# Optimization experiments

Measured on AMD Instinct MI355X. Metric: run time of the kernel, lower is better.

## Reference

```python
import jax, jax.numpy as jnp
import numpy as np

B, N, NF, EF, L = 32, 100, 128, 128, 3
ALPHA = 0.3  # keras LeakyReLU default


def _affine_act(h, W, S, Bb):
    # 1x1 conv (no bias) + folded BatchNorm (scale S, shift Bb) + LeakyReLU
    return jax.nn.leaky_relu(h @ W * S + Bb, ALPHA)


def _node_update(node_feat, edge_feat, W0, S0, B0, W1, S1, B1):
    n = node_feat.shape[1]
    dmask = (1.0 - jnp.eye(n, dtype=node_feat.dtype))[None, None]  # [1,1,N,N]
    ef = edge_feat * dmask
    norms = jnp.sum(jnp.abs(ef), axis=-1, keepdims=True)  # L1 norm
    ef = jnp.where(norms == 0, 0.0, ef / jnp.where(norms == 0, 1.0, norms))
    aggr = jnp.einsum('bemn,bnd->bemd', ef, node_feat)          # [B,2,N,D]
    aggr = jnp.concatenate([aggr[:, 0], aggr[:, 1]], axis=-1)   # [B,N,2D]
    x = jnp.concatenate([node_feat, aggr], axis=-1)             # [B,N,3D]
    h = _affine_act(x, W0, S0, B0)
    return _affine_act(h, W1, S1, B1)


def _edge_update(node_feat, edge_feat, convs, Wout, bout):
    n = node_feat.shape[1]
    # pairwise abs-diff: [B,N,N,F]
    h = jnp.abs(node_feat[:, :, None, :] - node_feat[:, None, :, :])
    for W, S, Bb in convs:
        h = _affine_act(h, W, S, Bb)
    sim = jax.nn.sigmoid(h @ Wout + bout)          # [B,N,N]
    sims = jnp.stack([sim, 1.0 - sim], axis=1)     # [B,2,N,N]
    eye = jnp.eye(n, dtype=node_feat.dtype)
    ef = edge_feat * (1.0 - eye)[None, None]
    merge_sum = jnp.sum(ef, axis=-1, keepdims=True)
    ef = ef * sims
    norms = jnp.sum(jnp.abs(ef), axis=-1, keepdims=True)
    ef = jnp.where(norms == 0, 0.0, ef / jnp.where(norms == 0, 1.0, norms))
    ef = ef * merge_sum
    force = jnp.stack([eye, jnp.zeros_like(eye)], axis=0)[None]  # [1,2,N,N]
    ef = ef + force + 1e-6
    return ef / jnp.sum(ef, axis=1, keepdims=True)


def setup_inputs() -> dict:
    key = jax.random.key(0)
    ks = jax.random.split(key, 10)
    f32 = jnp.float32

    def w(k, shape):
        return (jax.random.normal(k, shape, f32) * 0.05).astype(f32)

    d = {}
    d['node_feat'] = jax.random.normal(ks[0], (B, N, NF), f32)
    d['edge_feat'] = jax.random.uniform(ks[1], (B, 2, N, N), dtype=f32)
    # node-update MLP (ratio [2,1]): in 3*NF -> 2*NF -> NF
    d['nW0'] = w(ks[2], (L, 3 * NF, 2 * NF)); d['nS0'] = jnp.ones((L, 2 * NF), f32); d['nB0'] = jnp.zeros((L, 2 * NF), f32)
    d['nW1'] = w(ks[3], (L, 2 * NF, NF));     d['nS1'] = jnp.ones((L, NF), f32);     d['nB1'] = jnp.zeros((L, NF), f32)
    # edge sim network (ratio [2,2,1,1]): NF -> 2EF -> 2EF -> EF -> EF -> 1
    d['eW0'] = w(ks[4], (L, NF, 2 * EF));     d['eS0'] = jnp.ones((L, 2 * EF), f32); d['eB0'] = jnp.zeros((L, 2 * EF), f32)
    d['eW1'] = w(ks[5], (L, 2 * EF, 2 * EF)); d['eS1'] = jnp.ones((L, 2 * EF), f32); d['eB1'] = jnp.zeros((L, 2 * EF), f32)
    d['eW2'] = w(ks[6], (L, 2 * EF, EF));     d['eS2'] = jnp.ones((L, EF), f32);     d['eB2'] = jnp.zeros((L, EF), f32)
    d['eW3'] = w(ks[7], (L, EF, EF));         d['eS3'] = jnp.ones((L, EF), f32);     d['eB3'] = jnp.zeros((L, EF), f32)
    d['eWout'] = w(ks[8], (L, EF));           d['eBout'] = jnp.zeros((L,), f32)
    return d


def reference(node_feat, edge_feat, nW0, nS0, nB0, nW1, nS1, nB1,
              eW0, eS0, eB0, eW1, eS1, eB1, eW2, eS2, eB2, eW3, eS3, eB3,
              eWout, eBout):
    nf, ef = node_feat, edge_feat
    for l in range(L):
        nf = _node_update(nf, ef, nW0[l], nS0[l], nB0[l], nW1[l], nS1[l], nB1[l])
        convs = [(eW0[l], eS0[l], eB0[l]), (eW1[l], eS1[l], eB1[l]),
                 (eW2[l], eS2[l], eB2[l]), (eW3[l], eS3[l], eB3[l])]
        ef = _edge_update(nf, ef, convs, eWout[l], eBout[l])
    return ef
```

## Files before the change

### kernel.cpp

```cpp
#include <hip/hip_runtime.h>
#include <math.h>

#define ALPHA 0.3f

constexpr int B  = 32;
constexpr int N  = 100;
constexpr int NF = 128;
constexpr int L  = 3;
constexpr int NN = N * N;
constexpr int NTRI = N * (N + 1) / 2;
constexpr int NPAIR_TRI = B * NTRI;
constexpr int PT = 80;
constexpr int RT = 32;

typedef __attribute__((ext_vector_type(8))) short short8;
typedef __attribute__((ext_vector_type(4))) float f32x4;

__device__ __forceinline__ unsigned short f2bf(float x) {
    union { float f; unsigned u; } v; v.f = x;
    unsigned r = v.u + 0x7FFF + ((v.u >> 16) & 1);
    return (unsigned short)(r >> 16);
}
__device__ __forceinline__ float bf2f(unsigned short h) {
    union { unsigned u; float f; } v; v.u = ((unsigned)h) << 16;
    return v.f;
}
__device__ __forceinline__ unsigned cvt_pk(float lo, float hi) {
    unsigned r;
    asm("v_cvt_pk_bf16_f32 %0, %1, %2" : "=v"(r) : "v"(lo), "v"(hi));
    return r;
}

__device__ __forceinline__ void tri_decode(int t, int& io, int& jo) {
    int ii = (int)((201.0f - sqrtf(40401.0f - 8.0f * (float)t)) * 0.5f);
    ii = max(0, min(99, ii));
    while (ii > 0 && ii * (201 - ii) / 2 > t) --ii;
    while ((ii + 1) * (200 - ii) / 2 <= t) ++ii;
    io = ii;
    jo = ii + (t - ii * (201 - ii) / 2);
}

__device__ __forceinline__ void wprep_elem(const float* __restrict__ W,
                                           const float* __restrict__ S,
                                           unsigned short* __restrict__ Wp,
                                           int K, int C, int idx) {
    const int per = K * C;
    const int l = idx / per, r = idx - l * per;
    const int KS = K / 32;
    const int j    = r & 7;
    const int lane = (r >> 3) & 63;
    const int t2   = r >> 9;
    const int ks = t2 % KS, ct = t2 / KS;
    const int c = ct * 16 + (lane & 15);
    const int k = ks * 32 + (lane >> 4) * 8 + j;
    float v = W[(size_t)l * per + (size_t)k * C + c] * S[l * C + c];
    Wp[idx] = f2bf(v);
}

constexpr int SEG0 = L * 128 * 256;
constexpr int SEG1 = L * 256 * 256;
constexpr int SEG2 = L * 256 * 128;
constexpr int SEG3 = L * 128 * 128;
constexpr int SEG4 = L * 384 * 256;
constexpr int SEG5 = L * 256 * 128;
constexpr int PREP_TOTAL = SEG0 + SEG1 + SEG2 + SEG3 + SEG4 + SEG5 + NTRI;

__global__ void k_prep_all(
    const float* __restrict__ eW0, const float* __restrict__ eS0, unsigned short* __restrict__ w0t,
    const float* __restrict__ eW1, const float* __restrict__ eS1, unsigned short* __restrict__ w1t,
    const float* __restrict__ eW2, const float* __restrict__ eS2, unsigned short* __restrict__ w2t,
    const float* __restrict__ eW3, const float* __restrict__ eS3, unsigned short* __restrict__ w3t,
    const float* __restrict__ nW0, const float* __restrict__ nS0, unsigned short* __restrict__ nw0f,
    const float* __restrict__ nW1, const float* __restrict__ nS1, unsigned short* __restrict__ nw1f,
    unsigned* __restrict__ tab) {
    int idx = blockIdx.x * 256 + threadIdx.x;
    if (idx < SEG0) { wprep_elem(eW0, eS0, w0t, 128, 256, idx); return; }
    idx -= SEG0;
    if (idx < SEG1) { wprep_elem(eW1, eS1, w1t, 256, 256, idx); return; }
    idx -= SEG1;
    if (idx < SEG2) { wprep_elem(eW2, eS2, w2t, 256, 128, idx); return; }
    idx -= SEG2;
    if (idx < SEG3) { wprep_elem(eW3, eS3, w3t, 128, 128, idx); return; }
    idx -= SEG3;
    if (idx < SEG4) { wprep_elem(nW0, nS0, nw0f, 384, 256, idx); return; }
    idx -= SEG4;
    if (idx < SEG5) { wprep_elem(nW1, nS1, nw1f, 256, 128, idx); return; }
    idx -= SEG5;
    if (idx < NTRI) {
        int i, j;
        tri_decode(idx, i, j);
        tab[idx] = (unsigned)((i << 8) | j);
    }
}

__global__ void k_aggr_x(const float* __restrict__ nf,
                         const float* __restrict__ ef,
                         float* __restrict__ x) {
    const int b = blockIdx.x / N;
    const int m = blockIdx.x - b * N;
    const int t = threadIdx.x;

    __shared__ float w0[128], w1[128];

    float e0 = 0.f, e1 = 0.f;
    if (t < N) {
        e0 = ef[((size_t)(b * 2 + 0) * N + m) * N + t];
        e1 = ef[((size_t)(b * 2 + 1) * N + m) * N + t];
        if (t == m) { e0 = 0.f; e1 = 0.f; }
    }
    w0[t] = fabsf(e0);
    w1[t] = fabsf(e1);
    __syncthreads();
    for (int s = 64; s > 0; s >>= 1) {
        if (t < s) { w0[t] += w0[t + s]; w1[t] += w1[t + s]; }
        __syncthreads();
    }
    const float s0 = w0[0];
    const float s1 = w1[0];
    __syncthreads();
    w0[t] = (s0 == 0.f) ? 0.f : e0 / s0;
    w1[t] = (s1 == 0.f) ? 0.f : e1 / s1;
    __syncthreads();

    const float* nfb = nf + (size_t)b * N * NF;
    float a0 = 0.f, a1 = 0.f;
#pragma unroll 4
    for (int n = 0; n < N; ++n) {
        const float v = nfb[(size_t)n * NF + t];
        a0 = fmaf(w0[n], v, a0);
        a1 = fmaf(w1[n], v, a1);
    }
    float* xr = x + (size_t)(b * N + m) * (3 * NF);
    xr[t]          = nfb[(size_t)m * NF + t];
    xr[NF + t]     = a0;
    xr[2 * NF + t] = a1;
}

template <int K, int NT>
__device__ __forceinline__ void load_bv0(const unsigned short* __restrict__ Wf,
                                         int lane, int wave, short8* bv) {
    constexpr int KS = K / 32;
#pragma unroll
    for (int n = 0; n < NT; ++n)
        bv[n] = *(const short8*)(Wf + (((size_t)(wave * NT + n) * KS) * 64 + lane) * 8);
}

template <int K, int COUT, int NT, int MT>
__device__ __forceinline__ void layer_mfma(const unsigned short* in,
                                           unsigned short* out,
                                           const unsigned short* __restrict__ Wf,
                                           const float* __restrict__ Bb,
                                           int lane, int wave, const short8* bv0) {
    constexpr int KS = K / 32;
    const int r16 = lane & 15, g = lane >> 4;
    f32x4 acc[MT][NT];
#pragma unroll
    for (int n = 0; n < NT; ++n) {
        const f32x4 binit = *(const f32x4*)(Bb + (wave * NT + n) * 16 + g * 4);
#pragma unroll
        for (int m = 0; m < MT; ++m) acc[m][n] = binit;
    }

#pragma unroll
    for (int ks = 0; ks < KS; ++ks) {
        short8 av[MT];
        const int abyte = (ks * 64 + g * 16) ^ (r16 << 4);
#pragma unroll
        for (int m = 0; m < MT; ++m) {
            const int p = m * 16 + r16;
            av[m] = *(const short8*)((const char*)in + p * (K * 2) + abyte);
        }
        short8 bv[NT];
#pragma unroll
        for (int n = 0; n < NT; ++n) {
            if (ks == 0) bv[n] = bv0[n];
            else bv[n] = *(const short8*)(Wf + (((size_t)(wave * NT + n) * KS + ks) * 64 + lane) * 8);
        }
#pragma unroll
        for (int m = 0; m < MT; ++m)
#pragma unroll
            for (int n = 0; n < NT; ++n)
                acc[m][n] = __builtin_amdgcn_mfma_f32_16x16x32_bf16(
                    bv[n], av[m], acc[m][n], 0, 0, 0);
    }
#pragma unroll
    for (int n = 0; n < NT; ++n) {
        const int c0 = wave * NT * 16 + n * 16 + g * 4;
#pragma unroll
        for (int m = 0; m < MT; ++m) {
            const int p = m * 16 + r16;
            float v0 = acc[m][n][0]; v0 = fmaxf(v0, ALPHA * v0);
            float v1 = acc[m][n][1]; v1 = fmaxf(v1, ALPHA * v1);
            float v2 = acc[m][n][2]; v2 = fmaxf(v2, ALPHA * v2);
            float v3 = acc[m][n][3]; v3 = fmaxf(v3, ALPHA * v3);
            uint2 w;
            w.x = cvt_pk(v0, v1);
            w.y = cvt_pk(v2, v3);
            const int byte = (c0 * 2) ^ (r16 << 4);
            *(uint2*)((char*)out + p * (COUT * 2) + byte) = w;
        }
    }
}

template <int K, int MT>
__device__ __forceinline__ void layer_mfma_sim(const unsigned short* in,
                                               float* __restrict__ psum,
                                               const unsigned short* __restrict__ Wf,
                                               const float* __restrict__ Bb,
                                               const float* __restrict__ Wout,
                                               int lane, int wave, short8 bv0) {
    constexpr int KS = K / 32;
    const int r16 = lane & 15, g = lane >> 4;
    f32x4 acc[MT];
    {
        const f32x4 binit = *(const f32x4*)(Bb + wave * 16 + g * 4);
#pragma unroll
        for (int m = 0; m < MT; ++m) acc[m] = binit;
    }

#pragma unroll
    for (int ks = 0; ks < KS; ++ks) {
        short8 av[MT];
        const int abyte = (ks * 64 + g * 16) ^ (r16 << 4);
#pragma unroll
        for (int m = 0; m < MT; ++m) {
            const int p = m * 16 + r16;
            av[m] = *(const short8*)((const char*)in + p * (K * 2) + abyte);
        }
        const short8 bv = (ks == 0) ? bv0
            : *(const short8*)(Wf + (((size_t)wave * KS + ks) * 64 + lane) * 8);
#pragma unroll
        for (int m = 0; m < MT; ++m)
            acc[m] = __builtin_amdgcn_mfma_f32_16x16x32_bf16(bv, av[m], acc[m], 0, 0, 0);
    }

    const float4 w4 = *(const float4*)(Wout + wave * 16 + g * 4);
#pragma unroll
    for (int m = 0; m < MT; ++m) {
        float v0 = acc[m][0]; v0 = fmaxf(v0, ALPHA * v0);
        float v1 = acc[m][1]; v1 = fmaxf(v1, ALPHA * v1);
        float v2 = acc[m][2]; v2 = fmaxf(v2, ALPHA * v2);
        float v3 = acc[m][3]; v3 = fmaxf(v3, ALPHA * v3);
        float part = v0 * w4.x;
        part = fmaf(v1, w4.y, part);
        part = fmaf(v2, w4.z, part);
        part = fmaf(v3, w4.w, part);
        part += __shfl_xor(part, 16);
        part += __shfl_xor(part, 32);
        if (g == 0) psum[wave * (MT * 16) + m * 16 + r16] = part;
    }
}

template <int K, int COUT, int NT, int MT>
__device__ __forceinline__ void layer_mfma_f32out(const unsigned short* in,
                                                  float* __restrict__ outg, int row0,
                                                  const unsigned short* __restrict__ Wf,
                                                  const float* __restrict__ Bb,
                                                  int lane, int wave, const short8* bv0) {
    constexpr int KS = K / 32;
    const int r16 = lane & 15, g = lane >> 4;
    f32x4 acc[MT][NT];
#pragma unroll
    for (int n = 0; n < NT; ++n) {
        const f32x4 binit = *(const f32x4*)(Bb + (wave * NT + n) * 16 + g * 4);
#pragma unroll
        for (int m = 0; m < MT; ++m) acc[m][n] = binit;
    }

#pragma unroll
    for (int ks = 0; ks < KS; ++ks) {
        short8 av[MT];
        const int abyte = (ks * 64 + g * 16) ^ (r16 << 4);
#pragma unroll
        for (int m = 0; m < MT; ++m) {
            const int p = m * 16 + r16;
            av[m] = *(const short8*)((const char*)in + p * (K * 2) + abyte);
        }
        short8 bv[NT];
#pragma unroll
        for (int n = 0; n < NT; ++n) {
            if (ks == 0) bv[n] = bv0[n];
            else bv[n] = *(const short8*)(Wf + (((size_t)(wave * NT + n) * KS + ks) * 64 + lane) * 8);
        }
#pragma unroll
        for (int m = 0; m < MT; ++m)
#pragma unroll
            for (int n = 0; n < NT; ++n)
                acc[m][n] = __builtin_amdgcn_mfma_f32_16x16x32_bf16(
                    bv[n], av[m], acc[m][n], 0, 0, 0);
    }
#pragma unroll
    for (int n = 0; n < NT; ++n) {
        const int c0 = wave * NT * 16 + n * 16 + g * 4;
#pragma unroll
        for (int m = 0; m < MT; ++m) {
            const int p = m * 16 + r16;
            float4 o;
            o.x = acc[m][n][0]; o.x = fmaxf(o.x, ALPHA * o.x);
            o.y = acc[m][n][1]; o.y = fmaxf(o.y, ALPHA * o.y);
            o.z = acc[m][n][2]; o.z = fmaxf(o.z, ALPHA * o.z);
            o.w = acc[m][n][3]; o.w = fmaxf(o.w, ALPHA * o.w);
            *(float4*)(outg + (size_t)(row0 + p) * COUT + c0) = o;
        }
    }
}

__global__ __launch_bounds__(512, 4) void k_node_mfma(
    const float* __restrict__ x,
    const unsigned short* __restrict__ W0f, const float* __restrict__ B0,
    const unsigned short* __restrict__ W1f, const float* __restrict__ B1,
    float* __restrict__ nf_out) {
    __shared__ unsigned short bufA[RT * 384];
    __shared__ unsigned short bufB[RT * 256];
    const int t = threadIdx.x;
    const int lane = t & 63, wave = t >> 6;
    const int row0 = blockIdx.x * RT;

    {
        const int p = t >> 4, q = t & 15;
        const float* xr = x + (size_t)(row0 + p) * 384;
#pragma unroll
        for (int u = 0; u < 3; ++u) {
            const int q8 = q + u * 16;
            const float4 a0 = *(const float4*)(xr + q8 * 8);
            const float4 a1 = *(const float4*)(xr + q8 * 8 + 4);
            uint4 o;
            o.x = cvt_pk(a0.x, a0.y);
            o.y = cvt_pk(a0.z, a0.w);
            o.z = cvt_pk(a1.x, a1.y);
            o.w = cvt_pk(a1.z, a1.w);
            const int byte = (q8 * 16) ^ ((p & 15) << 4);
            *(uint4*)((char*)bufA + p * 768 + byte) = o;
        }
    }
    short8 bvp[2];
    load_bv0<384, 2>(W0f, lane, wave, bvp);
    __syncthreads();
    layer_mfma<384, 256, 2, 2>(bufA, bufB, W0f, B0, lane, wave, bvp);
    load_bv0<256, 1>(W1f, lane, wave, bvp);
    __syncthreads();
    layer_mfma_f32out<256, 128, 1, 2>(bufB, nf_out, row0, W1f, B1, lane, wave, bvp);
}

__global__ __launch_bounds__(512, 4) void k_pair_mlp_mfma(
    const float* __restrict__ nf,
    const unsigned short* __restrict__ W0f, const float* __restrict__ Bb0,
    const unsigned short* __restrict__ W1f, const float* __restrict__ Bb1,
    const unsigned short* __restrict__ W2f, const float* __restrict__ Bb2,
    const unsigned short* __restrict__ W3f, const float* __restrict__ Bb3,
    const float* __restrict__ Wout, const float* __restrict__ boutp,
    const unsigned* __restrict__ tab,
    float* __restrict__ sim) {
    __shared__ unsigned short bufA[PT * 256];
    __shared__ unsigned short bufB[PT * 256];
    const int t = threadIdx.x;
    const int lane = t & 63, wave = t >> 6;
    const int tile0 = blockIdx.x * PT;

    {
        const int p0 = t >> 4, q = t & 15;
        for (int p = p0; p < PT; p += 32) {
            const int P = tile0 + p;
            const int b = P / NTRI;
            const unsigned ij = tab[P - b * NTRI];
            const int i = ij >> 8, j = ij & 255;
            const float4* fi = (const float4*)(nf + ((size_t)(b * N + i)) * NF + q * 8);
            const float4* fj = (const float4*)(nf + ((size_t)(b * N + j)) * NF + q * 8);
            const float4 a0 = fi[0], a1 = fi[1];
            const float4 c0 = fj[0], c1 = fj[1];
            uint4 o;
            o.x = cvt_pk(fabsf(a0.x - c0.x), fabsf(a0.y - c0.y));
            o.y = cvt_pk(fabsf(a0.z - c0.z), fabsf(a0.w - c0.w));
            o.z = cvt_pk(fabsf(a1.x - c1.x), fabsf(a1.y - c1.y));
            o.w = cvt_pk(fabsf(a1.z - c1.z), fabsf(a1.w - c1.w));
            const int byte = (q * 16) ^ ((p & 15) << 4);
            *(uint4*)((char*)bufA + p * 256 + byte) = o;
        }
    }
    short8 bvp[2];
    load_bv0<128, 2>(W0f, lane, wave, bvp);
    __syncthreads();
    layer_mfma<128, 256, 2, 5>(bufA, bufB, W0f, Bb0, lane, wave, bvp);
    load_bv0<256, 2>(W1f, lane, wave, bvp);
    __syncthreads();
    layer_mfma<256, 256, 2, 5>(bufB, bufA, W1f, Bb1, lane, wave, bvp);
    load_bv0<256, 1>(W2f, lane, wave, bvp);
    __syncthreads();
    layer_mfma<256, 128, 1, 5>(bufA, bufB, W2f, Bb2, lane, wave, bvp);
    load_bv0<128, 1>(W3f, lane, wave, bvp);
    __syncthreads();
    float* psum = (float*)bufA;
    layer_mfma_sim<128, 5>(bufB, psum, W3f, Bb3, Wout, lane, wave, bvp[0]);
    __syncthreads();

    if (t < PT) {
        float acc = 0.f;
#pragma unroll
        for (int w = 0; w < 8; ++w) acc += psum[w * PT + t];
        const int P = tile0 + t;
        const int b = P / NTRI;
        const unsigned ij = tab[P - b * NTRI];
        const int i = ij >> 8, j = ij & 255;
        const float v = acc + boutp[0];
        const float sv = 1.f / (1.f + expf(-v));
        sim[((size_t)(b * N) + i) * N + j] = sv;
        sim[((size_t)(b * N) + j) * N + i] = sv;
    }
}

__global__ void k_edge_update(const float* __restrict__ ef_in,
                              const float* __restrict__ sim,
                              float* __restrict__ ef_out) {
    const int b = blockIdx.x / N;
    const int i = blockIdx.x - b * N;
    const int t = threadIdx.x;

    __shared__ float r0[128], r1[128], r2[128], r3[128];

    float e0 = 0.f, e1 = 0.f, s = 0.f;
    if (t < N) {
        e0 = ef_in[((size_t)(b * 2 + 0) * N + i) * N + t];
        e1 = ef_in[((size_t)(b * 2 + 1) * N + i) * N + t];
        if (t == i) { e0 = 0.f; e1 = 0.f; }
        s = sim[(size_t)(b * N + i) * N + t];
    }
    float f0 = e0 * s;
    float f1 = e1 * (1.f - s);
    r0[t] = e0; r1[t] = e1; r2[t] = fabsf(f0); r3[t] = fabsf(f1);
    __syncthreads();
    for (int st = 64; st > 0; st >>= 1) {
        if (t < st) {
            r0[t] += r0[t + st];
            r1[t] += r1[t + st];
            r2[t] += r2[t + st];
            r3[t] += r3[t + st];
        }
        __syncthreads();
    }
    const float m0 = r0[0], m1 = r1[0], n0 = r2[0], n1 = r3[0];
    if (t < N) {
        f0 = (n0 == 0.f) ? 0.f : (f0 / n0) * m0;
        f1 = (n1 == 0.f) ? 0.f : (f1 / n1) * m1;
        if (t == i) f0 += 1.f;
        f0 += 1e-6f;
        f1 += 1e-6f;
        const float inv = 1.f / (f0 + f1);
        ef_out[((size_t)(b * 2 + 0) * N + i) * N + t] = f0 * inv;
        ef_out[((size_t)(b * 2 + 1) * N + i) * N + t] = f1 * inv;
    }
}

__global__ void k_edge_aggr(const float* __restrict__ ef_in,
                            const float* __restrict__ sim,
                            const float* __restrict__ nf,
                            float* __restrict__ ef_out,
                            float* __restrict__ x) {
    const int b = blockIdx.x / N;
    const int i = blockIdx.x - b * N;
    const int t = threadIdx.x;

    __shared__ float r0[128], r1[128], r2[128], r3[128];
    __shared__ float w0s[128], w1s[128];

    float e0 = 0.f, e1 = 0.f, s = 0.f;
    if (t < N) {
        e0 = ef_in[((size_t)(b * 2 + 0) * N + i) * N + t];
        e1 = ef_in[((size_t)(b * 2 + 1) * N + i) * N + t];
        if (t == i) { e0 = 0.f; e1 = 0.f; }
        s = sim[(size_t)(b * N + i) * N + t];
    }
    float f0 = e0 * s;
    float f1 = e1 * (1.f - s);
    r0[t] = e0; r1[t] = e1; r2[t] = fabsf(f0); r3[t] = fabsf(f1);
    __syncthreads();
    for (int st = 64; st > 0; st >>= 1) {
        if (t < st) {
            r0[t] += r0[t + st];
            r1[t] += r1[t + st];
            r2[t] += r2[t + st];
            r3[t] += r3[t + st];
        }
        __syncthreads();
    }
    const float m0 = r0[0], m1 = r1[0], n0 = r2[0], n1 = r3[0];
    float g0 = 0.f, g1 = 0.f;
    if (t < N) {
        f0 = (n0 == 0.f) ? 0.f : (f0 / n0) * m0;
        f1 = (n1 == 0.f) ? 0.f : (f1 / n1) * m1;
        if (t == i) f0 += 1.f;
        f0 += 1e-6f;
        f1 += 1e-6f;
        const float inv = 1.f / (f0 + f1);
        g0 = f0 * inv;
        g1 = f1 * inv;
        ef_out[((size_t)(b * 2 + 0) * N + i) * N + t] = g0;
        ef_out[((size_t)(b * 2 + 1) * N + i) * N + t] = g1;
    }

    const float a0in = (t < N && t != i) ? g0 : 0.f;
    const float a1in = (t < N && t != i) ? g1 : 0.f;
    __syncthreads();
    r0[t] = fabsf(a0in);
    r1[t] = fabsf(a1in);
    __syncthreads();
    for (int st = 64; st > 0; st >>= 1) {
        if (t < st) { r0[t] += r0[t + st]; r1[t] += r1[t + st]; }
        __syncthreads();
    }
    const float s0 = r0[0], s1 = r1[0];
    __syncthreads();
    w0s[t] = (s0 == 0.f) ? 0.f : a0in / s0;
    w1s[t] = (s1 == 0.f) ? 0.f : a1in / s1;
    __syncthreads();

    const float* nfb = nf + (size_t)b * N * NF;
    float a0 = 0.f, a1 = 0.f;
#pragma unroll 4
    for (int n = 0; n < N; ++n) {
        const float v = nfb[(size_t)n * NF + t];
        a0 = fmaf(w0s[n], v, a0);
        a1 = fmaf(w1s[n], v, a1);
    }
    float* xr = x + (size_t)(b * N + i) * (3 * NF);
    xr[t]          = nfb[(size_t)i * NF + t];
    xr[NF + t]     = a0;
    xr[2 * NF + t] = a1;
}

extern "C" void kernel_launch(void* const* d_in, const int* in_sizes, int n_in,
                              void* d_out, int out_size, void* d_ws, size_t ws_size,
                              hipStream_t stream) {
    (void)in_sizes; (void)n_in; (void)out_size; (void)ws_size;

    const float* node_feat = (const float*)d_in[0];
    const float* edge_feat = (const float*)d_in[1];
    const float* nW0 = (const float*)d_in[2];
    const float* nS0 = (const float*)d_in[3];
    const float* nB0 = (const float*)d_in[4];
    const float* nW1 = (const float*)d_in[5];
    const float* nS1 = (const float*)d_in[6];
    const float* nB1 = (const float*)d_in[7];
    const float* eW0 = (const float*)d_in[8];
    const float* eS0 = (const float*)d_in[9];
    const float* eB0 = (const float*)d_in[10];
    const float* eW1 = (const float*)d_in[11];
    const float* eS1 = (const float*)d_in[12];
    const float* eB1 = (const float*)d_in[13];
    const float* eW2 = (const float*)d_in[14];
    const float* eS2 = (const float*)d_in[15];
    const float* eB2 = (const float*)d_in[16];
    const float* eW3 = (const float*)d_in[17];
    const float* eS3 = (const float*)d_in[18];
    const float* eB3 = (const float*)d_in[19];
    const float* eWout = (const float*)d_in[20];
    const float* eBout = (const float*)d_in[21];

    float* ws     = (float*)d_ws;
    float* nf_a   = ws;
    float* nf_b   = nf_a + (size_t)B * N * NF;
    float* xbuf   = nf_b + (size_t)B * N * NF;
    float* ef_ws  = xbuf + (size_t)B * N * 3 * NF;
    float* simbuf = ef_ws + (size_t)B * 2 * N * N;
    unsigned short* w0t = (unsigned short*)(simbuf + (size_t)B * N * N);
    unsigned short* w1t = w0t + (size_t)L * 256 * 128;
    unsigned short* w2t = w1t + (size_t)L * 256 * 256;
    unsigned short* w3t = w2t + (size_t)L * 128 * 256;
    unsigned short* nw0f = w3t + (size_t)L * 128 * 128;
    unsigned short* nw1f = nw0f + (size_t)L * 256 * 384;
    unsigned* tab = (unsigned*)(nw1f + (size_t)L * 128 * 256);

    k_prep_all<<<(PREP_TOTAL + 255) / 256, 256, 0, stream>>>(
        eW0, eS0, w0t, eW1, eS1, w1t, eW2, eS2, w2t, eW3, eS3, w3t,
        nW0, nS0, nw0f, nW1, nS1, nw1f, tab);

    const float* ef_cur = edge_feat;
    float* nf_next_buf[3] = {nf_a, nf_b, nf_a};

    k_aggr_x<<<B * N, 128, 0, stream>>>(node_feat, edge_feat, xbuf);

    for (int l = 0; l < L; ++l) {
        k_node_mfma<<<B * N / RT, 512, 0, stream>>>(
            xbuf,
            nw0f + (size_t)l * 256 * 384, nB0 + l * 2 * NF,
            nw1f + (size_t)l * 128 * 256, nB1 + l * NF,
            nf_next_buf[l]);
        const float* nf_cur = nf_next_buf[l];

        k_pair_mlp_mfma<<<NPAIR_TRI / PT, 512, 0, stream>>>(
            nf_cur,
            w0t + (size_t)l * 256 * 128, eB0 + l * 256,
            w1t + (size_t)l * 256 * 256, eB1 + l * 256,
            w2t + (size_t)l * 128 * 256, eB2 + l * 128,
            w3t + (size_t)l * 128 * 128, eB3 + l * 128,
            eWout + (size_t)l * 128, eBout + l, tab, simbuf);

        if (l < L - 1) {
            k_edge_aggr<<<B * N, 128, 0, stream>>>(
                ef_cur, simbuf, nf_cur, ef_ws, xbuf);
            ef_cur = ef_ws;
        } else {
            k_edge_update<<<B * N, 128, 0, stream>>>(ef_cur, simbuf, (float*)d_out);
        }
    }
}
```

Measured before the change: 229.9 us.

## Retile pair-MLP waves into a 2x4 grid and shrink the pair tile

The pair MLP kernel now handles 64 pairs per block instead of 80. Its 8 waves form a 2x4 grid over row and column tiles, where each wave previously covered all row tiles for a slice of output columns. Each wave now reads fewer activation fragments from LDS but more weight fragments from global memory, and the final sigmoid reduction is reworked to sum over column-wave partials. The smaller tile lowers LDS use and gives exactly divisible blocks, but weight-load traffic per MFMA goes up.

```diff
diff --git a/kernel.cpp b/kernel.cpp
--- a/kernel.cpp
+++ b/kernel.cpp
@@ -10,7 +10,7 @@
 constexpr int NN = N * N;
 constexpr int NTRI = N * (N + 1) / 2;
 constexpr int NPAIR_TRI = B * NTRI;
-constexpr int PT = 80;
+constexpr int PT = 64;
 constexpr int RT = 32;
 
 typedef __attribute__((ext_vector_type(8))) short short8;
@@ -138,11 +138,11 @@
 
 template <int K, int NT>
 __device__ __forceinline__ void load_bv0(const unsigned short* __restrict__ Wf,
-                                         int lane, int wave, short8* bv) {
+                                         int lane, int ct0, short8* bv) {
     constexpr int KS = K / 32;
 #pragma unroll
     for (int n = 0; n < NT; ++n)
-        bv[n] = *(const short8*)(Wf + (((size_t)(wave * NT + n) * KS) * 64 + lane) * 8);
+        bv[n] = *(const short8*)(Wf + (((size_t)(ct0 + n) * KS) * 64 + lane) * 8);
 }
 
 template <int K, int COUT, int NT, int MT>
@@ -150,13 +150,14 @@
                                            unsigned short* out,
                                            const unsigned short* __restrict__ Wf,
                                            const float* __restrict__ Bb,
-                                           int lane, int wave, const short8* bv0) {
+                                           int lane, int mbase, int ct0,
+                                           const short8* bv0) {
     constexpr int KS = K / 32;
     const int r16 = lane & 15, g = lane >> 4;
     f32x4 acc[MT][NT];
 #pragma unroll
     for (int n = 0; n < NT; ++n) {
-        const f32x4 binit = *(const f32x4*)(Bb + (wave * NT + n) * 16 + g * 4);
+        const f32x4 binit = *(const f32x4*)(Bb + (ct0 + n) * 16 + g * 4);
 #pragma unroll
         for (int m = 0; m < MT; ++m) acc[m][n] = binit;
     }
@@ -167,14 +168,14 @@
         const int abyte = (ks * 64 + g * 16) ^ (r16 << 4);
 #pragma unroll
         for (int m = 0; m < MT; ++m) {
-            const int p = m * 16 + r16;
+            const int p = (mbase + m) * 16 + r16;
             av[m] = *(const short8*)((const char*)in + p * (K * 2) + abyte);
         }
         short8 bv[NT];
 #pragma unroll
         for (int n = 0; n < NT; ++n) {
             if (ks == 0) bv[n] = bv0[n];
-            else bv[n] = *(const short8*)(Wf + (((size_t)(wave * NT + n) * KS + ks) * 64 + lane) * 8);
+            else bv[n] = *(const short8*)(Wf + (((size_t)(ct0 + n) * KS + ks) * 64 + lane) * 8);
         }
 #pragma unroll
         for (int m = 0; m < MT; ++m)
@@ -185,10 +186,10 @@
     }
 #pragma unroll
     for (int n = 0; n < NT; ++n) {
-        const int c0 = wave * NT * 16 + n * 16 + g * 4;
+        const int c0 = (ct0 + n) * 16 + g * 4;
 #pragma unroll
         for (int m = 0; m < MT; ++m) {
-            const int p = m * 16 + r16;
+            const int p = (mbase + m) * 16 + r16;
             float v0 = acc[m][n][0]; v0 = fmaxf(v0, ALPHA * v0);
             float v1 = acc[m][n][1]; v1 = fmaxf(v1, ALPHA * v1);
             float v2 = acc[m][n][2]; v2 = fmaxf(v2, ALPHA * v2);
@@ -202,20 +203,22 @@
     }
 }
 
-template <int K, int MT>
+template <int K, int NT, int MT>
 __device__ __forceinline__ void layer_mfma_sim(const unsigned short* in,
                                                float* __restrict__ psum,
                                                const unsigned short* __restrict__ Wf,
                                                const float* __restrict__ Bb,
                                                const float* __restrict__ Wout,
-                                               int lane, int wave, short8 bv0) {
+                                               int lane, int mbase, int ct0, int wave,
+                                               const short8* bv0) {
     constexpr int KS = K / 32;
     const int r16 = lane & 15, g = lane >> 4;
-    f32x4 acc[MT];
-    {
-        const f32x4 binit = *(const f32x4*)(Bb + wave * 16 + g * 4);
-#pragma unroll
-        for (int m = 0; m < MT; ++m) acc[m] = binit;
+    f32x4 acc[MT][NT];
+#pragma unroll
+    for (int n = 0; n < NT; ++n) {
+        const f32x4 binit = *(const f32x4*)(Bb + (ct0 + n) * 16 + g * 4);
+#pragma unroll
+        for (int m = 0; m < MT; ++m) acc[m][n] = binit;
     }
 
 #pragma unroll
@@ -224,27 +227,41 @@
         const int abyte = (ks * 64 + g * 16) ^ (r16 << 4);
 #pragma unroll
         for (int m = 0; m < MT; ++m) {
-            const int p = m * 16 + r16;
+            const int p = (mbase + m) * 16 + r16;
             av[m] = *(const short8*)((const char*)in + p * (K * 2) + abyte);
         }
-        const short8 bv = (ks == 0) ? bv0
-            : *(const short8*)(Wf + (((size_t)wave * KS + ks) * 64 + lane) * 8);
+        short8 bv[NT];
+#pragma unroll
+        for (int n = 0; n < NT; ++n) {
+            if (ks == 0) bv[n] = bv0[n];
+            else bv[n] = *(const short8*)(Wf + (((size_t)(ct0 + n) * KS + ks) * 64 + lane) * 8);
+        }
 #pragma unroll
         for (int m = 0; m < MT; ++m)
-            acc[m] = __builtin_amdgcn_mfma_f32_16x16x32_bf16(bv, av[m], acc[m], 0, 0, 0);
-    }
-
-    const float4 w4 = *(const float4*)(Wout + wave * 16 + g * 4);
+#pragma unroll
+            for (int n = 0; n < NT; ++n)
+                acc[m][n] = __builtin_amdgcn_mfma_f32_16x16x32_bf16(
+                    bv[n], av[m], acc[m][n], 0, 0, 0);
+    }
+
+    float4 w4[NT];
+#pragma unroll
+    for (int n = 0; n < NT; ++n)
+        w4[n] = *(const float4*)(Wout + (ct0 + n) * 16 + g * 4);
 #pragma unroll
     for (int m = 0; m < MT; ++m) {
-        float v0 = acc[m][0]; v0 = fmaxf(v0, ALPHA * v0);
-        float v1 = acc[m][1]; v1 = fmaxf(v1, ALPHA * v1);
-        float v2 = acc[m][2]; v2 = fmaxf(v2, ALPHA * v2);
-        float v3 = acc[m][3]; v3 = fmaxf(v3, ALPHA * v3);
-        float part = v0 * w4.x;
-        part = fmaf(v1, w4.y, part);
-        part = fmaf(v2, w4.z, part);
-        part = fmaf(v3, w4.w, part);
+        float part = 0.f;
+#pragma unroll
+        for (int n = 0; n < NT; ++n) {
+            float v0 = acc[m][n][0]; v0 = fmaxf(v0, ALPHA * v0);
+            float v1 = acc[m][n][1]; v1 = fmaxf(v1, ALPHA * v1);
+            float v2 = acc[m][n][2]; v2 = fmaxf(v2, ALPHA * v2);
+            float v3 = acc[m][n][3]; v3 = fmaxf(v3, ALPHA * v3);
+            part = fmaf(v0, w4[n].x, part);
+            part = fmaf(v1, w4[n].y, part);
+            part = fmaf(v2, w4[n].z, part);
+            part = fmaf(v3, w4[n].w, part);
+        }
         part += __shfl_xor(part, 16);
         part += __shfl_xor(part, 32);
         if (g == 0) psum[wave * (MT * 16) + m * 16 + r16] = part;
@@ -256,13 +273,14 @@
                                                   float* __restrict__ outg, int row0,
                                                   const unsigned short* __restrict__ Wf,
                                                   const float* __restrict__ Bb,
-                                                  int lane, int wave, const short8* bv0) {
+                                                  int lane, int mbase, int ct0,
+                                                  const short8* bv0) {
     constexpr int KS = K / 32;
     const int r16 = lane & 15, g = lane >> 4;
     f32x4 acc[MT][NT];
 #pragma unroll
     for (int n = 0; n < NT; ++n) {
-        const f32x4 binit = *(const f32x4*)(Bb + (wave * NT + n) * 16 + g * 4);
+        const f32x4 binit = *(const f32x4*)(Bb + (ct0 + n) * 16 + g * 4);
 #pragma unroll
         for (int m = 0; m < MT; ++m) acc[m][n] = binit;
     }
@@ -273,14 +291,14 @@
         const int abyte = (ks * 64 + g * 16) ^ (r16 << 4);
 #pragma unroll
         for (int m = 0; m < MT; ++m) {
-            const int p = m * 16 + r16;
+            const int p = (mbase + m) * 16 + r16;
             av[m] = *(const short8*)((const char*)in + p * (K * 2) + abyte);
         }
         short8 bv[NT];
 #pragma unroll
         for (int n = 0; n < NT; ++n) {
             if (ks == 0) bv[n] = bv0[n];
-            else bv[n] = *(const short8*)(Wf + (((size_t)(wave * NT + n) * KS + ks) * 64 + lane) * 8);
+            else bv[n] = *(const short8*)(Wf + (((size_t)(ct0 + n) * KS + ks) * 64 + lane) * 8);
         }
 #pragma unroll
         for (int m = 0; m < MT; ++m)
@@ -291,10 +309,10 @@
     }
 #pragma unroll
     for (int n = 0; n < NT; ++n) {
-        const int c0 = wave * NT * 16 + n * 16 + g * 4;
+        const int c0 = (ct0 + n) * 16 + g * 4;
 #pragma unroll
         for (int m = 0; m < MT; ++m) {
-            const int p = m * 16 + r16;
+            const int p = (mbase + m) * 16 + r16;
             float4 o;
             o.x = acc[m][n][0]; o.x = fmaxf(o.x, ALPHA * o.x);
             o.y = acc[m][n][1]; o.y = fmaxf(o.y, ALPHA * o.y);
@@ -333,13 +351,13 @@
             *(uint4*)((char*)bufA + p * 768 + byte) = o;
         }
     }
-    short8 bvp[2];
-    load_bv0<384, 2>(W0f, lane, wave, bvp);
-    __syncthreads();
-    layer_mfma<384, 256, 2, 2>(bufA, bufB, W0f, B0, lane, wave, bvp);
+    short8 bvp[4];
+    load_bv0<384, 2>(W0f, lane, wave * 2, bvp);
+    __syncthreads();
+    layer_mfma<384, 256, 2, 2>(bufA, bufB, W0f, B0, lane, 0, wave * 2, bvp);
     load_bv0<256, 1>(W1f, lane, wave, bvp);
     __syncthreads();
-    layer_mfma_f32out<256, 128, 1, 2>(bufB, nf_out, row0, W1f, B1, lane, wave, bvp);
+    layer_mfma_f32out<256, 128, 1, 2>(bufB, nf_out, row0, W1f, B1, lane, 0, wave, bvp);
 }
 
 __global__ __launch_bounds__(512, 4) void k_pair_mlp_mfma(
@@ -355,11 +373,15 @@
     __shared__ unsigned short bufB[PT * 256];
     const int t = threadIdx.x;
     const int lane = t & 63, wave = t >> 6;
+    const int wm = wave >> 2;
+    const int wn = wave & 3;
     const int tile0 = blockIdx.x * PT;
 
     {
         const int p0 = t >> 4, q = t & 15;
-        for (int p = p0; p < PT; p += 32) {
+#pragma unroll
+        for (int pp = 0; pp < 2; ++pp) {
+            const int p = p0 + pp * 32;
             const int P = tile0 + p;
             const int b = P / NTRI;
             const unsigned ij = tab[P - b * NTRI];
@@ -377,26 +399,27 @@
             *(uint4*)((char*)bufA + p * 256 + byte) = o;
         }
     }
-    short8 bvp[2];
-    load_bv0<128, 2>(W0f, lane, wave, bvp);
-    __syncthreads();
-    layer_mfma<128, 256, 2, 5>(bufA, bufB, W0f, Bb0, lane, wave, bvp);
-    load_bv0<256, 2>(W1f, lane, wave, bvp);
-    __syncthreads();
-    layer_mfma<256, 256, 2, 5>(bufB, bufA, W1f, Bb1, lane, wave, bvp);
-    load_bv0<256, 1>(W2f, lane, wave, bvp);
-    __syncthreads();
-    layer_mfma<256, 128, 1, 5>(bufA, bufB, W2f, Bb2, lane, wave, bvp);
-    load_bv0<128, 1>(W3f, lane, wave, bvp);
+    short8 bvp[4];
+    load_bv0<128, 4>(W0f, lane, wn * 4, bvp);
+    __syncthreads();
+    layer_mfma<128, 256, 4, 2>(bufA, bufB, W0f, Bb0, lane, wm * 2, wn * 4, bvp);
+    load_bv0<256, 4>(W1f, lane, wn * 4, bvp);
+    __syncthreads();
+    layer_mfma<256, 256, 4, 2>(bufB, bufA, W1f, Bb1, lane, wm * 2, wn * 4, bvp);
+    load_bv0<256, 2>(W2f, lane, wn * 2, bvp);
+    __syncthreads();
+    layer_mfma<256, 128, 2, 2>(bufA, bufB, W2f, Bb2, lane, wm * 2, wn * 2, bvp);
+    load_bv0<128, 2>(W3f, lane, wn * 2, bvp);
     __syncthreads();
     float* psum = (float*)bufA;
-    layer_mfma_sim<128, 5>(bufB, psum, W3f, Bb3, Wout, lane, wave, bvp[0]);
+    layer_mfma_sim<128, 2, 2>(bufB, psum, W3f, Bb3, Wout, lane, wm * 2, wn * 2, wave, bvp);
     __syncthreads();
 
     if (t < PT) {
+        const int pwm = t >> 5, lp = t & 31;
         float acc = 0.f;
 #pragma unroll
-        for (int w = 0; w < 8; ++w) acc += psum[w * PT + t];
+        for (int w = 0; w < 4; ++w) acc += psum[(pwm * 4 + w) * 32 + lp];
         const int P = tile0 + t;
         const int b = P / NTRI;
         const unsigned ij = tab[P - b * NTRI];
```

After: 268.2 us. 1.17x slower.
